# Kernel tuning notes

Measured on AMD Instinct MI355X. Metric: run time of the kernel, lower is better.

Reference implementation:

```python
import jax, jax.numpy as jnp
import numpy as np

D_MODEL = 2048
N_ROOMS = 128
B = 128
S = 512


def setup_inputs() -> dict:
    key = jax.random.key(0)
    ks = jax.random.split(key, 8)
    scale = 1.0 / np.sqrt(D_MODEL)
    x = jax.random.normal(ks[0], (B, S, D_MODEL), dtype=jnp.float32)
    room_summaries = jax.random.normal(ks[1], (N_ROOMS, D_MODEL), dtype=jnp.float32)
    Wc = jax.random.uniform(ks[2], (D_MODEL, D_MODEL), minval=-scale, maxval=scale, dtype=jnp.float32)
    bc = jax.random.uniform(ks[3], (D_MODEL,), minval=-scale, maxval=scale, dtype=jnp.float32)
    Ww = jax.random.uniform(ks[4], (N_ROOMS * N_ROOMS, D_MODEL), minval=-scale, maxval=scale, dtype=jnp.float32)
    bw = jax.random.uniform(ks[5], (N_ROOMS * N_ROOMS,), minval=-scale, maxval=scale, dtype=jnp.float32)
    adjacency = jnp.eye(N_ROOMS, dtype=jnp.float32) + jax.random.normal(ks[6], (N_ROOMS, N_ROOMS), dtype=jnp.float32) * 0.1
    return {"x": x, "room_summaries": room_summaries, "Wc": Wc, "bc": bc,
            "Ww": Ww, "bw": bw, "adjacency": adjacency}


def reference(x, room_summaries, Wc, bc, Ww, bw, adjacency):
    n_rooms = room_summaries.shape[0]
    # context: mean over seq then linear -> [B, d_model]
    context = jnp.mean(x, axis=1) @ Wc.T + bc
    # dynamic warp of adjacency -> [B, N, N]
    warp = (context @ Ww.T + bw).reshape(-1, n_rooms, n_rooms) * 0.1
    adj = jax.nn.softmax(adjacency[None, :, :] + warp, axis=-1)
    # raw room scores: [B, N]
    raw_scores = context @ room_summaries.T
    # adjacency-warped scores: [B, N]
    warped_scores = jnp.einsum('bij,bj->bi', adj, raw_scores)
    return jax.nn.sigmoid(warped_scores)
```

## Files before the change

kernel.cpp:

```cpp
#include <hip/hip_runtime.h>
#include <stdint.h>

#define D_MODEL 2048
#define N_ROOMS 128
#define BATCH   128
#define SEQ     512
#define NN      (N_ROOMS * N_ROOMS)

typedef short bf16x8 __attribute__((ext_vector_type(8)));
typedef float f32x4  __attribute__((ext_vector_type(4)));

__device__ __forceinline__ unsigned short f2bf(float f) {
    union { float f; uint32_t u; } c; c.f = f;
    uint32_t u = c.u;
    uint32_t r = (u + 0x7fffu + ((u >> 16) & 1u)) >> 16;
    return (unsigned short)r;
}
__device__ __forceinline__ float bf2f(unsigned short h) {
    union { uint32_t u; float f; } c; c.u = ((uint32_t)h) << 16;
    return c.f;
}

__global__ void k_mean_partial(const float* __restrict__ x, float* __restrict__ part) {
    int bx = blockIdx.x;
    int b = bx >> 3, rem = bx & 7;
    int sc = rem >> 1, dc = rem & 1;
    int d = dc * 1024 + threadIdx.x * 4;
    const float* p = x + ((size_t)(b * SEQ + sc * 128)) * D_MODEL + d;
    float ax = 0.f, ay = 0.f, az = 0.f, aw = 0.f;
    #pragma unroll 4
    for (int s = 0; s < 128; ++s) {
        float4 v = *(const float4*)p;
        ax += v.x; ay += v.y; az += v.z; aw += v.w;
        p += D_MODEL;
    }
    float4 o = {ax, ay, az, aw};
    *(float4*)(part + ((size_t)(sc * BATCH + b)) * D_MODEL + d) = o;
}

__global__ void k_mean_combine(const float* __restrict__ part, float* __restrict__ mean,
                               unsigned short* __restrict__ mhi, unsigned short* __restrict__ mlo) {
    int i = (blockIdx.x * 256 + threadIdx.x) * 4;
    float4 s = {0.f, 0.f, 0.f, 0.f};
    #pragma unroll
    for (int sc = 0; sc < 4; ++sc) {
        float4 v = *(const float4*)(part + (size_t)sc * BATCH * D_MODEL + i);
        s.x += v.x; s.y += v.y; s.z += v.z; s.w += v.w;
    }
    const float inv = 1.0f / (float)SEQ;
    s.x *= inv; s.y *= inv; s.z *= inv; s.w *= inv;
    *(float4*)(mean + i) = s;
    unsigned short h0 = f2bf(s.x), h1 = f2bf(s.y), h2 = f2bf(s.z), h3 = f2bf(s.w);
    ushort4 hv = {h0, h1, h2, h3};
    ushort4 lv = {f2bf(s.x - bf2f(h0)), f2bf(s.y - bf2f(h1)),
                  f2bf(s.z - bf2f(h2)), f2bf(s.w - bf2f(h3))};
    *(ushort4*)(mhi + i) = hv;
    *(ushort4*)(mlo + i) = lv;
}

__launch_bounds__(256)
__global__ void k_ctx_gemm(const unsigned short* __restrict__ mhi,
                           const unsigned short* __restrict__ mlo,
                           const float* __restrict__ Wc,
                           float* __restrict__ ctx_part) {
    __shared__ short Ah[128 * 72];
    __shared__ short Al[128 * 72];
    __shared__ short Bh[64 * 72];
    __shared__ short Bl[64 * 72];
    int bx = blockIdx.x;
    int nt = bx & 31, ks = bx >> 5;
    int n0 = nt * 64;
    int k0 = ks * 256;
    int tid = threadIdx.x, lane = tid & 63, w = tid >> 6;
    int mbase = w * 32;
    f32x4 acc[2][4] = {};
    for (int kt = 0; kt < 4; ++kt) {
        int kb = k0 + kt * 64;
        __syncthreads();
        #pragma unroll
        for (int i = 0; i < 4; ++i) {
            int u = tid + 256 * i;
            int row = u >> 3, c = u & 7;
            *(int4*)&Ah[row * 72 + c * 8] = *(const int4*)(mhi + (size_t)row * D_MODEL + kb + c * 8);
            *(int4*)&Al[row * 72 + c * 8] = *(const int4*)(mlo + (size_t)row * D_MODEL + kb + c * 8);
        }
        #pragma unroll
        for (int i = 0; i < 4; ++i) {
            int u = tid + 256 * i;
            int row = u >> 4, c = u & 15;
            float4 v = *(const float4*)(Wc + (size_t)(n0 + row) * D_MODEL + kb + c * 4);
            unsigned short h0 = f2bf(v.x), h1 = f2bf(v.y), h2 = f2bf(v.z), h3 = f2bf(v.w);
            ushort4 hv = {h0, h1, h2, h3};
            ushort4 lv = {f2bf(v.x - bf2f(h0)), f2bf(v.y - bf2f(h1)),
                          f2bf(v.z - bf2f(h2)), f2bf(v.w - bf2f(h3))};
            *(ushort4*)&Bh[row * 72 + c * 4] = hv;
            *(ushort4*)&Bl[row * 72 + c * 4] = lv;
        }
        __syncthreads();
        #pragma unroll
        for (int kk = 0; kk < 64; kk += 32) {
            int ko = kk + (lane >> 4) * 8;
            int mr = mbase + (lane & 15);
            bf16x8 ah0 = *(const bf16x8*)&Ah[mr * 72 + ko];
            bf16x8 ah1 = *(const bf16x8*)&Ah[(mr + 16) * 72 + ko];
            bf16x8 al0 = *(const bf16x8*)&Al[mr * 72 + ko];
            bf16x8 al1 = *(const bf16x8*)&Al[(mr + 16) * 72 + ko];
            #pragma unroll
            for (int ni = 0; ni < 4; ++ni) {
                int nr = ni * 16 + (lane & 15);
                bf16x8 bh = *(const bf16x8*)&Bh[nr * 72 + ko];
                bf16x8 bl = *(const bf16x8*)&Bl[nr * 72 + ko];
                acc[0][ni] = __builtin_amdgcn_mfma_f32_16x16x32_bf16(ah0, bh, acc[0][ni], 0, 0, 0);
                acc[0][ni] = __builtin_amdgcn_mfma_f32_16x16x32_bf16(al0, bh, acc[0][ni], 0, 0, 0);
                acc[0][ni] = __builtin_amdgcn_mfma_f32_16x16x32_bf16(ah0, bl, acc[0][ni], 0, 0, 0);
                acc[1][ni] = __builtin_amdgcn_mfma_f32_16x16x32_bf16(ah1, bh, acc[1][ni], 0, 0, 0);
                acc[1][ni] = __builtin_amdgcn_mfma_f32_16x16x32_bf16(al1, bh, acc[1][ni], 0, 0, 0);
                acc[1][ni] = __builtin_amdgcn_mfma_f32_16x16x32_bf16(ah1, bl, acc[1][ni], 0, 0, 0);
            }
        }
    }
    int col = lane & 15, quad = lane >> 4;
    #pragma unroll
    for (int mi = 0; mi < 2; ++mi)
        #pragma unroll
        for (int ni = 0; ni < 4; ++ni)
            #pragma unroll
            for (int r = 0; r < 4; ++r) {
                int m = mbase + mi * 16 + quad * 4 + r;
                int n = n0 + ni * 16 + col;
                ctx_part[((size_t)(ks * BATCH + m)) * D_MODEL + n] = acc[mi][ni][r];
            }
}

__global__ void k_ctx_finalize(const float* __restrict__ ctx_part, const float* __restrict__ bc,
                               float* __restrict__ ctx, unsigned short* __restrict__ ctxb) {
    int i = (blockIdx.x * 256 + threadIdx.x) * 4;
    float4 s = {0.f, 0.f, 0.f, 0.f};
    #pragma unroll
    for (int ks = 0; ks < 8; ++ks) {
        float4 v = *(const float4*)(ctx_part + (size_t)ks * BATCH * D_MODEL + i);
        s.x += v.x; s.y += v.y; s.z += v.z; s.w += v.w;
    }
    int d = i & (D_MODEL - 1);
    float4 bias = *(const float4*)(bc + d);
    s.x += bias.x; s.y += bias.y; s.z += bias.z; s.w += bias.w;
    *(float4*)(ctx + i) = s;
    ushort4 hv = {f2bf(s.x), f2bf(s.y), f2bf(s.z), f2bf(s.w)};
    *(ushort4*)(ctxb + i) = hv;
}

__global__ void k_raw(const float* __restrict__ ctx, const float* __restrict__ room,
                      float* __restrict__ raw) {
    __shared__ float ct[16][132];
    __shared__ float rt[16][132];
    int bg = blockIdx.x >> 3, ng = blockIdx.x & 7;
    int tid = threadIdx.x;
    int bi = tid >> 4, ni = tid & 15;
    float acc = 0.f;
    for (int kc = 0; kc < D_MODEL; kc += 128) {
        __syncthreads();
        #pragma unroll
        for (int i = 0; i < 2; ++i) {
            int u = tid + 256 * i;
            int row = u >> 5, c = u & 31;
            *(float4*)&ct[row][c * 4] = *(const float4*)(ctx + (size_t)(bg * 16 + row) * D_MODEL + kc + c * 4);
            *(float4*)&rt[row][c * 4] = *(const float4*)(room + (size_t)(ng * 16 + row) * D_MODEL + kc + c * 4);
        }
        __syncthreads();
        #pragma unroll 8
        for (int c = 0; c < 32; ++c) {
            float4 a = *(const float4*)&ct[bi][c * 4];
            float4 r = *(const float4*)&rt[ni][c * 4];
            acc += a.x * r.x + a.y * r.y + a.z * r.z + a.w * r.w;
        }
    }
    raw[(bg * 16 + bi) * N_ROOMS + ng * 16 + ni] = acc;
}

__launch_bounds__(256)
__global__ void k_warp_gemm(const unsigned short* __restrict__ ctxb,
                            const float* __restrict__ Ww,
                            float* __restrict__ wp) {
    __shared__ short A[128 * 72];
    __shared__ short Bt[64 * 72];
    int bx = blockIdx.x;
    int nt = bx & 255, ks = bx >> 8;
    int n0 = nt * 64;
    int k0 = ks * 1024;
    int tid = threadIdx.x, lane = tid & 63, w = tid >> 6;
    int mbase = w * 32;
    f32x4 acc[2][4] = {};
    for (int kt = 0; kt < 16; ++kt) {
        int kb = k0 + kt * 64;
        __syncthreads();
        #pragma unroll
        for (int i = 0; i < 4; ++i) {
            int u = tid + 256 * i;
            int row = u >> 3, c = u & 7;
            *(int4*)&A[row * 72 + c * 8] = *(const int4*)(ctxb + (size_t)row * D_MODEL + kb + c * 8);
        }
        #pragma unroll
        for (int i = 0; i < 4; ++i) {
            int u = tid + 256 * i;
            int row = u >> 4, c = u & 15;
            float4 v = *(const float4*)(Ww + (size_t)(n0 + row) * D_MODEL + kb + c * 4);
            ushort4 hv = {f2bf(v.x), f2bf(v.y), f2bf(v.z), f2bf(v.w)};
            *(ushort4*)&Bt[row * 72 + c * 4] = hv;
        }
        __syncthreads();
        #pragma unroll
        for (int kk = 0; kk < 64; kk += 32) {
            int ko = kk + (lane >> 4) * 8;
            int mr = mbase + (lane & 15);
            bf16x8 a0 = *(const bf16x8*)&A[mr * 72 + ko];
            bf16x8 a1 = *(const bf16x8*)&A[(mr + 16) * 72 + ko];
            #pragma unroll
            for (int ni = 0; ni < 4; ++ni) {
                bf16x8 bfr = *(const bf16x8*)&Bt[(ni * 16 + (lane & 15)) * 72 + ko];
                acc[0][ni] = __builtin_amdgcn_mfma_f32_16x16x32_bf16(a0, bfr, acc[0][ni], 0, 0, 0);
                acc[1][ni] = __builtin_amdgcn_mfma_f32_16x16x32_bf16(a1, bfr, acc[1][ni], 0, 0, 0);
            }
        }
    }
    int col = lane & 15, quad = lane >> 4;
    #pragma unroll
    for (int mi = 0; mi < 2; ++mi)
        #pragma unroll
        for (int ni = 0; ni < 4; ++ni)
            #pragma unroll
            for (int r = 0; r < 4; ++r) {
                int m = mbase + mi * 16 + quad * 4 + r;
                int n = n0 + ni * 16 + col;
                wp[(size_t)ks * BATCH * NN + (size_t)m * NN + n] = acc[mi][ni][r];
            }
}

__global__ void k_epilogue(const float* __restrict__ wp, const float* __restrict__ bw,
                           const float* __restrict__ adj, const float* __restrict__ raw,
                           float* __restrict__ out) {
    int tid = threadIdx.x, lane = tid & 63, w = tid >> 6;
    int row = blockIdx.x * 4 + w;
    int b = row >> 7, i = row & 127;
    int j0 = lane, j1 = lane + 64;
    size_t base = (size_t)row * 128;
    float w0 = wp[base + j0] + wp[(size_t)BATCH * NN + base + j0];
    float w1 = wp[base + j1] + wp[(size_t)BATCH * NN + base + j1];
    float l0 = adj[i * 128 + j0] + 0.1f * (w0 + bw[i * 128 + j0]);
    float l1 = adj[i * 128 + j1] + 0.1f * (w1 + bw[i * 128 + j1]);
    float m = fmaxf(l0, l1);
    #pragma unroll
    for (int off = 32; off; off >>= 1) m = fmaxf(m, __shfl_xor(m, off));
    float p0 = __expf(l0 - m), p1 = __expf(l1 - m);
    float s = p0 + p1;
    float t = p0 * raw[b * 128 + j0] + p1 * raw[b * 128 + j1];
    #pragma unroll
    for (int off = 32; off; off >>= 1) { s += __shfl_xor(s, off); t += __shfl_xor(t, off); }
    if (lane == 0) out[row] = 1.0f / (1.0f + __expf(-(t / s)));
}

extern "C" void kernel_launch(void* const* d_in, const int* in_sizes, int n_in,
                              void* d_out, int out_size, void* d_ws, size_t ws_size,
                              hipStream_t stream) {
    (void)in_sizes; (void)n_in; (void)out_size; (void)ws_size;
    const float* x    = (const float*)d_in[0];
    const float* room = (const float*)d_in[1];
    const float* Wc   = (const float*)d_in[2];
    const float* bc   = (const float*)d_in[3];
    const float* Ww   = (const float*)d_in[4];
    const float* bw   = (const float*)d_in[5];
    const float* adj  = (const float*)d_in[6];
    float* out = (float*)d_out;
    char* ws = (char*)d_ws;
    const size_t MB = 1u << 20;
    float*          part     = (float*)(ws + 0);
    float*          mean     = (float*)(ws + 4 * MB);
    unsigned short* mhi      = (unsigned short*)(ws + 5 * MB);
    unsigned short* mlo      = (unsigned short*)(ws + 5 * MB + 512 * 1024);
    float*          ctx_part = (float*)(ws + 6 * MB);
    float*          ctx      = (float*)(ws + 14 * MB);
    unsigned short* ctxb     = (unsigned short*)(ws + 15 * MB);
    float*          raw      = (float*)(ws + 15 * MB + 512 * 1024);
    float*          wp       = (float*)(ws + 16 * MB);

    hipLaunchKernelGGL(k_mean_partial, dim3(1024), dim3(256), 0, stream, x, part);
    hipLaunchKernelGGL(k_mean_combine, dim3(256), dim3(256), 0, stream, part, mean, mhi, mlo);
    hipLaunchKernelGGL(k_ctx_gemm, dim3(256), dim3(256), 0, stream, mhi, mlo, Wc, ctx_part);
    hipLaunchKernelGGL(k_ctx_finalize, dim3(256), dim3(256), 0, stream, ctx_part, bc, ctx, ctxb);
    hipLaunchKernelGGL(k_raw, dim3(64), dim3(256), 0, stream, ctx, room, raw);
    hipLaunchKernelGGL(k_warp_gemm, dim3(512), dim3(256), 0, stream, ctxb, Ww, wp);
    hipLaunchKernelGGL(k_epilogue, dim3(4096), dim3(256), 0, stream, wp, bw, adj, raw, out);
}
```

Measured before the change: 860.8 us.

## Fold raw-score GEMM into warp GEMM, drop split-bf16 context GEMM, double mean parallelism

```diff
diff --git a/kernel.cpp b/kernel.cpp
--- a/kernel.cpp
+++ b/kernel.cpp
@@ -6,6 +6,7 @@
 #define BATCH   128
 #define SEQ     512
 #define NN      (N_ROOMS * N_ROOMS)
+#define NCOL    (NN + N_ROOMS)
 
 typedef short bf16x8 __attribute__((ext_vector_type(8)));
 typedef float f32x4  __attribute__((ext_vector_type(4)));
@@ -16,20 +17,16 @@
     uint32_t r = (u + 0x7fffu + ((u >> 16) & 1u)) >> 16;
     return (unsigned short)r;
 }
-__device__ __forceinline__ float bf2f(unsigned short h) {
-    union { uint32_t u; float f; } c; c.u = ((uint32_t)h) << 16;
-    return c.f;
-}
 
 __global__ void k_mean_partial(const float* __restrict__ x, float* __restrict__ part) {
     int bx = blockIdx.x;
-    int b = bx >> 3, rem = bx & 7;
+    int b = bx >> 4, rem = bx & 15;
     int sc = rem >> 1, dc = rem & 1;
     int d = dc * 1024 + threadIdx.x * 4;
-    const float* p = x + ((size_t)(b * SEQ + sc * 128)) * D_MODEL + d;
+    const float* p = x + ((size_t)(b * SEQ + sc * 64)) * D_MODEL + d;
     float ax = 0.f, ay = 0.f, az = 0.f, aw = 0.f;
-    #pragma unroll 4
-    for (int s = 0; s < 128; ++s) {
+    #pragma unroll 8
+    for (int s = 0; s < 64; ++s) {
         float4 v = *(const float4*)p;
         ax += v.x; ay += v.y; az += v.z; aw += v.w;
         p += D_MODEL;
@@ -38,35 +35,26 @@
     *(float4*)(part + ((size_t)(sc * BATCH + b)) * D_MODEL + d) = o;
 }
 
-__global__ void k_mean_combine(const float* __restrict__ part, float* __restrict__ mean,
-                               unsigned short* __restrict__ mhi, unsigned short* __restrict__ mlo) {
+__global__ void k_mean_combine(const float* __restrict__ part,
+                               unsigned short* __restrict__ meanb) {
     int i = (blockIdx.x * 256 + threadIdx.x) * 4;
     float4 s = {0.f, 0.f, 0.f, 0.f};
     #pragma unroll
-    for (int sc = 0; sc < 4; ++sc) {
+    for (int sc = 0; sc < 8; ++sc) {
         float4 v = *(const float4*)(part + (size_t)sc * BATCH * D_MODEL + i);
         s.x += v.x; s.y += v.y; s.z += v.z; s.w += v.w;
     }
     const float inv = 1.0f / (float)SEQ;
-    s.x *= inv; s.y *= inv; s.z *= inv; s.w *= inv;
-    *(float4*)(mean + i) = s;
-    unsigned short h0 = f2bf(s.x), h1 = f2bf(s.y), h2 = f2bf(s.z), h3 = f2bf(s.w);
-    ushort4 hv = {h0, h1, h2, h3};
-    ushort4 lv = {f2bf(s.x - bf2f(h0)), f2bf(s.y - bf2f(h1)),
-                  f2bf(s.z - bf2f(h2)), f2bf(s.w - bf2f(h3))};
-    *(ushort4*)(mhi + i) = hv;
-    *(ushort4*)(mlo + i) = lv;
+    ushort4 hv = {f2bf(s.x * inv), f2bf(s.y * inv), f2bf(s.z * inv), f2bf(s.w * inv)};
+    *(ushort4*)(meanb + i) = hv;
 }
 
 __launch_bounds__(256)
-__global__ void k_ctx_gemm(const unsigned short* __restrict__ mhi,
-                           const unsigned short* __restrict__ mlo,
+__global__ void k_ctx_gemm(const unsigned short* __restrict__ meanb,
                            const float* __restrict__ Wc,
                            float* __restrict__ ctx_part) {
-    __shared__ short Ah[128 * 72];
-    __shared__ short Al[128 * 72];
-    __shared__ short Bh[64 * 72];
-    __shared__ short Bl[64 * 72];
+    __shared__ short A[128 * 72];
+    __shared__ short Bt[64 * 72];
     int bx = blockIdx.x;
     int nt = bx & 31, ks = bx >> 5;
     int n0 = nt * 64;
@@ -81,41 +69,28 @@
         for (int i = 0; i < 4; ++i) {
             int u = tid + 256 * i;
             int row = u >> 3, c = u & 7;
-            *(int4*)&Ah[row * 72 + c * 8] = *(const int4*)(mhi + (size_t)row * D_MODEL + kb + c * 8);
-            *(int4*)&Al[row * 72 + c * 8] = *(const int4*)(mlo + (size_t)row * D_MODEL + kb + c * 8);
+            *(int4*)&A[row * 72 + c * 8] = *(const int4*)(meanb + (size_t)row * D_MODEL + kb + c * 8);
         }
         #pragma unroll
         for (int i = 0; i < 4; ++i) {
             int u = tid + 256 * i;
             int row = u >> 4, c = u & 15;
             float4 v = *(const float4*)(Wc + (size_t)(n0 + row) * D_MODEL + kb + c * 4);
-            unsigned short h0 = f2bf(v.x), h1 = f2bf(v.y), h2 = f2bf(v.z), h3 = f2bf(v.w);
-            ushort4 hv = {h0, h1, h2, h3};
-            ushort4 lv = {f2bf(v.x - bf2f(h0)), f2bf(v.y - bf2f(h1)),
-                          f2bf(v.z - bf2f(h2)), f2bf(v.w - bf2f(h3))};
-            *(ushort4*)&Bh[row * 72 + c * 4] = hv;
-            *(ushort4*)&Bl[row * 72 + c * 4] = lv;
+            ushort4 hv = {f2bf(v.x), f2bf(v.y), f2bf(v.z), f2bf(v.w)};
+            *(ushort4*)&Bt[row * 72 + c * 4] = hv;
         }
         __syncthreads();
         #pragma unroll
         for (int kk = 0; kk < 64; kk += 32) {
             int ko = kk + (lane >> 4) * 8;
             int mr = mbase + (lane & 15);
-            bf16x8 ah0 = *(const bf16x8*)&Ah[mr * 72 + ko];
-            bf16x8 ah1 = *(const bf16x8*)&Ah[(mr + 16) * 72 + ko];
-            bf16x8 al0 = *(const bf16x8*)&Al[mr * 72 + ko];
-            bf16x8 al1 = *(const bf16x8*)&Al[(mr + 16) * 72 + ko];
+            bf16x8 a0 = *(const bf16x8*)&A[mr * 72 + ko];
+            bf16x8 a1 = *(const bf16x8*)&A[(mr + 16) * 72 + ko];
             #pragma unroll
             for (int ni = 0; ni < 4; ++ni) {
-                int nr = ni * 16 + (lane & 15);
-                bf16x8 bh = *(const bf16x8*)&Bh[nr * 72 + ko];
-                bf16x8 bl = *(const bf16x8*)&Bl[nr * 72 + ko];
-                acc[0][ni] = __builtin_amdgcn_mfma_f32_16x16x32_bf16(ah0, bh, acc[0][ni], 0, 0, 0);
-                acc[0][ni] = __builtin_amdgcn_mfma_f32_16x16x32_bf16(al0, bh, acc[0][ni], 0, 0, 0);
-                acc[0][ni] = __builtin_amdgcn_mfma_f32_16x16x32_bf16(ah0, bl, acc[0][ni], 0, 0, 0);
-                acc[1][ni] = __builtin_amdgcn_mfma_f32_16x16x32_bf16(ah1, bh, acc[1][ni], 0, 0, 0);
-                acc[1][ni] = __builtin_amdgcn_mfma_f32_16x16x32_bf16(al1, bh, acc[1][ni], 0, 0, 0);
-                acc[1][ni] = __builtin_amdgcn_mfma_f32_16x16x32_bf16(ah1, bl, acc[1][ni], 0, 0, 0);
+                bf16x8 bfr = *(const bf16x8*)&Bt[(ni * 16 + (lane & 15)) * 72 + ko];
+                acc[0][ni] = __builtin_amdgcn_mfma_f32_16x16x32_bf16(a0, bfr, acc[0][ni], 0, 0, 0);
+                acc[1][ni] = __builtin_amdgcn_mfma_f32_16x16x32_bf16(a1, bfr, acc[1][ni], 0, 0, 0);
             }
         }
     }
@@ -133,7 +108,7 @@
 }
 
 __global__ void k_ctx_finalize(const float* __restrict__ ctx_part, const float* __restrict__ bc,
-                               float* __restrict__ ctx, unsigned short* __restrict__ ctxb) {
+                               unsigned short* __restrict__ ctxb) {
     int i = (blockIdx.x * 256 + threadIdx.x) * 4;
     float4 s = {0.f, 0.f, 0.f, 0.f};
     #pragma unroll
@@ -143,50 +118,23 @@
     }
     int d = i & (D_MODEL - 1);
     float4 bias = *(const float4*)(bc + d);
-    s.x += bias.x; s.y += bias.y; s.z += bias.z; s.w += bias.w;
-    *(float4*)(ctx + i) = s;
-    ushort4 hv = {f2bf(s.x), f2bf(s.y), f2bf(s.z), f2bf(s.w)};
+    ushort4 hv = {f2bf(s.x + bias.x), f2bf(s.y + bias.y), f2bf(s.z + bias.z), f2bf(s.w + bias.w)};
     *(ushort4*)(ctxb + i) = hv;
-}
-
-__global__ void k_raw(const float* __restrict__ ctx, const float* __restrict__ room,
-                      float* __restrict__ raw) {
-    __shared__ float ct[16][132];
-    __shared__ float rt[16][132];
-    int bg = blockIdx.x >> 3, ng = blockIdx.x & 7;
-    int tid = threadIdx.x;
-    int bi = tid >> 4, ni = tid & 15;
-    float acc = 0.f;
-    for (int kc = 0; kc < D_MODEL; kc += 128) {
-        __syncthreads();
-        #pragma unroll
-        for (int i = 0; i < 2; ++i) {
-            int u = tid + 256 * i;
-            int row = u >> 5, c = u & 31;
-            *(float4*)&ct[row][c * 4] = *(const float4*)(ctx + (size_t)(bg * 16 + row) * D_MODEL + kc + c * 4);
-            *(float4*)&rt[row][c * 4] = *(const float4*)(room + (size_t)(ng * 16 + row) * D_MODEL + kc + c * 4);
-        }
-        __syncthreads();
-        #pragma unroll 8
-        for (int c = 0; c < 32; ++c) {
-            float4 a = *(const float4*)&ct[bi][c * 4];
-            float4 r = *(const float4*)&rt[ni][c * 4];
-            acc += a.x * r.x + a.y * r.y + a.z * r.z + a.w * r.w;
-        }
-    }
-    raw[(bg * 16 + bi) * N_ROOMS + ng * 16 + ni] = acc;
 }
 
 __launch_bounds__(256)
 __global__ void k_warp_gemm(const unsigned short* __restrict__ ctxb,
                             const float* __restrict__ Ww,
+                            const float* __restrict__ room,
                             float* __restrict__ wp) {
     __shared__ short A[128 * 72];
     __shared__ short Bt[64 * 72];
     int bx = blockIdx.x;
-    int nt = bx & 255, ks = bx >> 8;
+    int nt = bx % 258, ks = bx / 258;
     int n0 = nt * 64;
     int k0 = ks * 1024;
+    const float* Bsrc = (nt < 256) ? (Ww + (size_t)n0 * D_MODEL)
+                                   : (room + (size_t)(n0 - NN) * D_MODEL);
     int tid = threadIdx.x, lane = tid & 63, w = tid >> 6;
     int mbase = w * 32;
     f32x4 acc[2][4] = {};
@@ -203,7 +151,7 @@
         for (int i = 0; i < 4; ++i) {
             int u = tid + 256 * i;
             int row = u >> 4, c = u & 15;
-            float4 v = *(const float4*)(Ww + (size_t)(n0 + row) * D_MODEL + kb + c * 4);
+            float4 v = *(const float4*)(Bsrc + (size_t)row * D_MODEL + kb + c * 4);
             ushort4 hv = {f2bf(v.x), f2bf(v.y), f2bf(v.z), f2bf(v.w)};
             *(ushort4*)&Bt[row * 72 + c * 4] = hv;
         }
@@ -231,30 +179,33 @@
             for (int r = 0; r < 4; ++r) {
                 int m = mbase + mi * 16 + quad * 4 + r;
                 int n = n0 + ni * 16 + col;
-                wp[(size_t)ks * BATCH * NN + (size_t)m * NN + n] = acc[mi][ni][r];
+                wp[((size_t)(ks * BATCH + m)) * NCOL + n] = acc[mi][ni][r];
             }
 }
 
 __global__ void k_epilogue(const float* __restrict__ wp, const float* __restrict__ bw,
-                           const float* __restrict__ adj, const float* __restrict__ raw,
-                           float* __restrict__ out) {
+                           const float* __restrict__ adj, float* __restrict__ out) {
     int tid = threadIdx.x, lane = tid & 63, w = tid >> 6;
     int row = blockIdx.x * 4 + w;
     int b = row >> 7, i = row & 127;
     int j0 = lane, j1 = lane + 64;
-    size_t base = (size_t)row * 128;
-    float w0 = wp[base + j0] + wp[(size_t)BATCH * NN + base + j0];
-    float w1 = wp[base + j1] + wp[(size_t)BATCH * NN + base + j1];
-    float l0 = adj[i * 128 + j0] + 0.1f * (w0 + bw[i * 128 + j0]);
-    float l1 = adj[i * 128 + j1] + 0.1f * (w1 + bw[i * 128 + j1]);
+    size_t b0 = (size_t)b * NCOL;
+    size_t b1 = (size_t)(BATCH + b) * NCOL;
+    int off = i * 128;
+    float w0 = wp[b0 + off + j0] + wp[b1 + off + j0];
+    float w1 = wp[b0 + off + j1] + wp[b1 + off + j1];
+    float r0 = wp[b0 + NN + j0] + wp[b1 + NN + j0];
+    float r1 = wp[b0 + NN + j1] + wp[b1 + NN + j1];
+    float l0 = adj[off + j0] + 0.1f * (w0 + bw[off + j0]);
+    float l1 = adj[off + j1] + 0.1f * (w1 + bw[off + j1]);
     float m = fmaxf(l0, l1);
     #pragma unroll
-    for (int off = 32; off; off >>= 1) m = fmaxf(m, __shfl_xor(m, off));
+    for (int o = 32; o; o >>= 1) m = fmaxf(m, __shfl_xor(m, o));
     float p0 = __expf(l0 - m), p1 = __expf(l1 - m);
     float s = p0 + p1;
-    float t = p0 * raw[b * 128 + j0] + p1 * raw[b * 128 + j1];
-    #pragma unroll
-    for (int off = 32; off; off >>= 1) { s += __shfl_xor(s, off); t += __shfl_xor(t, off); }
+    float t = p0 * r0 + p1 * r1;
+    #pragma unroll
+    for (int o = 32; o; o >>= 1) { s += __shfl_xor(s, o); t += __shfl_xor(t, o); }
     if (lane == 0) out[row] = 1.0f / (1.0f + __expf(-(t / s)));
 }
 
@@ -273,20 +224,15 @@
     char* ws = (char*)d_ws;
     const size_t MB = 1u << 20;
     float*          part     = (float*)(ws + 0);
-    float*          mean     = (float*)(ws + 4 * MB);
-    unsigned short* mhi      = (unsigned short*)(ws + 5 * MB);
-    unsigned short* mlo      = (unsigned short*)(ws + 5 * MB + 512 * 1024);
-    float*          ctx_part = (float*)(ws + 6 * MB);
-    float*          ctx      = (float*)(ws + 14 * MB);
-    unsigned short* ctxb     = (unsigned short*)(ws + 15 * MB);
-    float*          raw      = (float*)(ws + 15 * MB + 512 * 1024);
-    float*          wp       = (float*)(ws + 16 * MB);
-
-    hipLaunchKernelGGL(k_mean_partial, dim3(1024), dim3(256), 0, stream, x, part);
-    hipLaunchKernelGGL(k_mean_combine, dim3(256), dim3(256), 0, stream, part, mean, mhi, mlo);
-    hipLaunchKernelGGL(k_ctx_gemm, dim3(256), dim3(256), 0, stream, mhi, mlo, Wc, ctx_part);
-    hipLaunchKernelGGL(k_ctx_finalize, dim3(256), dim3(256), 0, stream, ctx_part, bc, ctx, ctxb);
-    hipLaunchKernelGGL(k_raw, dim3(64), dim3(256), 0, stream, ctx, room, raw);
-    hipLaunchKernelGGL(k_warp_gemm, dim3(512), dim3(256), 0, stream, ctxb, Ww, wp);
-    hipLaunchKernelGGL(k_epilogue, dim3(4096), dim3(256), 0, stream, wp, bw, adj, raw, out);
-}
+    unsigned short* meanb    = (unsigned short*)(ws + 8 * MB);
+    float*          ctx_part = (float*)(ws + 9 * MB);
+    unsigned short* ctxb     = (unsigned short*)(ws + 17 * MB);
+    float*          wp       = (float*)(ws + 18 * MB);
+
+    hipLaunchKernelGGL(k_mean_partial, dim3(2048), dim3(256), 0, stream, x, part);
+    hipLaunchKernelGGL(k_mean_combine, dim3(256), dim3(256), 0, stream, part, meanb);
+    hipLaunchKernelGGL(k_ctx_gemm, dim3(256), dim3(256), 0, stream, meanb, Wc, ctx_part);
+    hipLaunchKernelGGL(k_ctx_finalize, dim3(256), dim3(256), 0, stream, ctx_part, bc, ctxb);
+    hipLaunchKernelGGL(k_warp_gemm, dim3(516), dim3(256), 0, stream, ctxb, Ww, room, wp);
+    hipLaunchKernelGGL(k_epilogue, dim3(4096), dim3(256), 0, stream, wp, bw, adj, out);
+}
```

Measured after the change: 840.3 us. -2.4%, faster.
